# Kernel tuning notes

Hardware: AMD Instinct MI355X
Metric: run time of the kernel (lower is better)

The kernel has to match this reference:

```python
import jax, jax.numpy as jnp
import numpy as np

DIM = 1024
HEADS = 16
EPS = 1e-5


def layer_norm(x, gamma, beta):
    mu = jnp.mean(x, axis=-1, keepdims=True)
    var = jnp.mean(jnp.square(x - mu), axis=-1, keepdims=True)
    return (x - mu) * jax.lax.rsqrt(var + EPS) * gamma + beta


def setup_inputs() -> dict:
    key = jax.random.key(0)
    ks = jax.random.split(key, 9)
    B, Nq, Nk = 8, 1024, 1024
    s = 1.0 / np.sqrt(DIM)
    return {
        "x": jax.random.normal(ks[0], (B, Nq, DIM), jnp.float32),
        "context": jax.random.normal(ks[1], (B, Nk, DIM), jnp.float32),
        "relative_position_bias": jax.random.normal(ks[2], (HEADS, Nq, Nk), jnp.float32),
        "Wq": jax.random.normal(ks[3], (DIM, DIM), jnp.float32) * s,
        "Wk": jax.random.normal(ks[4], (DIM, DIM), jnp.float32) * s,
        "Wv": jax.random.normal(ks[5], (DIM, DIM), jnp.float32) * s,
        "Wo": jax.random.normal(ks[6], (DIM, DIM), jnp.float32) * s,
        "bo": jnp.zeros((DIM,), jnp.float32),
        "gamma": jnp.ones((DIM,), jnp.float32),
        "beta": jnp.zeros((DIM,), jnp.float32),
    }


def reference(x, context, relative_position_bias, Wq, Wk, Wv, Wo, bo, gamma, beta):
    h = HEADS
    d = DIM // h
    scale = d ** -0.5
    xn = layer_norm(x, gamma, beta)
    cn = layer_norm(context, gamma, beta)
    B, Nq, _ = x.shape
    Nk = context.shape[1]
    # b n (h d) -> b h n d
    q = (xn @ Wq).reshape(B, Nq, h, d).transpose(0, 2, 1, 3)
    k = (cn @ Wk).reshape(B, Nk, h, d).transpose(0, 2, 1, 3)
    v = (cn @ Wv).reshape(B, Nk, h, d).transpose(0, 2, 1, 3)
    scores = jnp.einsum('bhid,bhjd->bhij', q, k) * scale
    scores = scores + relative_position_bias[None]
    attn = jax.nn.softmax(scores, axis=-1)
    out = jnp.einsum('bhij,bhjd->bhid', attn, v)
    out = out.transpose(0, 2, 1, 3).reshape(B, Nq, h * d)
    return out @ Wo + bo
```

## Files before the change

### kernel.cpp

```cpp
#include <hip/hip_runtime.h>
#include <hip/hip_bf16.h>
#include <stdint.h>

#define DIM   1024
#define HEADS 16
#define HD    64
#define NB    8
#define NTOK  1024
#define MROWS (NB*NTOK)

#define LOG2E 1.4426950408889634f
#define SCL   (0.125f * LOG2E)

typedef __attribute__((ext_vector_type(8))) _Float16 f16x8;
typedef __attribute__((ext_vector_type(4))) _Float16 f16x4;
typedef __attribute__((ext_vector_type(4))) float    f32x4;

typedef unsigned int uint_as1 __attribute__((address_space(1)));
typedef unsigned int uint_as3 __attribute__((address_space(3)));

__device__ __forceinline__ void gload16(const void* g, void* l) {
    __builtin_amdgcn_global_load_lds((const uint_as1*)g, (uint_as3*)l, 16, 0, 0);
}

__device__ __forceinline__ unsigned pkrtz(float a, float b) {
    auto h = __builtin_amdgcn_cvt_pkrtz(a, b);
    return __builtin_bit_cast(unsigned, h);
}

#if __has_builtin(__builtin_amdgcn_permlane32_swap)
__device__ __forceinline__ void swap32(unsigned& a, unsigned& b) {
    auto r = __builtin_amdgcn_permlane32_swap(a, b, false, false);
    a = r[0]; b = r[1];
}
#else
__device__ __forceinline__ void swap32(unsigned& a, unsigned& b) {
    unsigned as = (unsigned)__shfl_xor((int)a, 32, 64);
    unsigned bs = (unsigned)__shfl_xor((int)b, 32, 64);
    bool lo = ((threadIdx.x & 63) < 32);
    unsigned na = lo ? a : bs, nb = lo ? as : b;
    a = na; b = nb;
}
#endif
#if __has_builtin(__builtin_amdgcn_permlane16_swap)
__device__ __forceinline__ void swap16(unsigned& a, unsigned& b) {
    auto r = __builtin_amdgcn_permlane16_swap(a, b, false, false);
    a = r[0]; b = r[1];
}
#else
__device__ __forceinline__ void swap16(unsigned& a, unsigned& b) {
    unsigned as = (unsigned)__shfl_xor((int)a, 16, 64);
    unsigned bs = (unsigned)__shfl_xor((int)b, 16, 64);
    bool ev = ((threadIdx.x & 16) == 0);
    unsigned na = ev ? a : bs, nb = ev ? as : b;
    a = na; b = nb;
}
#endif
__device__ __forceinline__ float redsum32(float x) {
    unsigned a = __builtin_bit_cast(unsigned, x), b = a;
    swap32(a, b);
    return __builtin_bit_cast(float, a) + __builtin_bit_cast(float, b);
}
__device__ __forceinline__ float redsum16(float x) {
    unsigned a = __builtin_bit_cast(unsigned, x), b = a;
    swap16(a, b);
    return __builtin_bit_cast(float, a) + __builtin_bit_cast(float, b);
}

__global__ __launch_bounds__(256) void ln_kernel(const float* __restrict__ x,
                                                 const float* __restrict__ ctx,
                                                 const float* __restrict__ gamma,
                                                 const float* __restrict__ beta,
                                                 _Float16* __restrict__ xn,
                                                 _Float16* __restrict__ cn) {
    int row = blockIdx.x;
    const float* src; _Float16* dst;
    if (row < MROWS) { src = x + (size_t)row * DIM;          dst = xn + (size_t)row * DIM; }
    else             { int r = row - MROWS;
                       src = ctx + (size_t)r * DIM;          dst = cn + (size_t)r * DIM; }
    int t = threadIdx.x;
    float4 v = *(const float4*)(src + t * 4);
    float s  = v.x + v.y + v.z + v.w;
    float s2 = v.x*v.x + v.y*v.y + v.z*v.z + v.w*v.w;
    #pragma unroll
    for (int o = 32; o; o >>= 1) { s += __shfl_xor(s, o, 64); s2 += __shfl_xor(s2, o, 64); }
    __shared__ float red[8];
    int w = t >> 6, l = t & 63;
    if (l == 0) { red[w] = s; red[4 + w] = s2; }
    __syncthreads();
    s  = red[0] + red[1] + red[2] + red[3];
    s2 = red[4] + red[5] + red[6] + red[7];
    float mu   = s * (1.0f / DIM);
    float rstd = rsqrtf(s2 * (1.0f / DIM) - mu * mu + 1e-5f);
    float4 g  = *(const float4*)(gamma + t * 4);
    float4 bb = *(const float4*)(beta  + t * 4);
    f16x4 o;
    o[0] = (_Float16)((v.x - mu) * rstd * g.x + bb.x);
    o[1] = (_Float16)((v.y - mu) * rstd * g.y + bb.y);
    o[2] = (_Float16)((v.z - mu) * rstd * g.z + bb.z);
    o[3] = (_Float16)((v.w - mu) * rstd * g.w + bb.w);
    *(f16x4*)(dst + t * 4) = o;
}

__global__ __launch_bounds__(256) void biasconv_kernel(const float* __restrict__ bias,
                                                       _Float16* __restrict__ bias2) {
    size_t i = ((size_t)blockIdx.x * 256 + threadIdx.x) * 8;
    float4 a = *(const float4*)(bias + i);
    float4 b = *(const float4*)(bias + i + 4);
    f16x8 o;
    o[0] = (_Float16)(a.x * LOG2E); o[1] = (_Float16)(a.y * LOG2E);
    o[2] = (_Float16)(a.z * LOG2E); o[3] = (_Float16)(a.w * LOG2E);
    o[4] = (_Float16)(b.x * LOG2E); o[5] = (_Float16)(b.y * LOG2E);
    o[6] = (_Float16)(b.z * LOG2E); o[7] = (_Float16)(b.w * LOG2E);
    *(f16x8*)(bias2 + i) = o;
}

__global__ __launch_bounds__(256) void wtrans_kernel(const float* __restrict__ Wq, const float* __restrict__ Wk,
                                                     const float* __restrict__ Wv, const float* __restrict__ Wo,
                                                     _Float16* __restrict__ Tq, _Float16* __restrict__ Tk,
                                                     _Float16* __restrict__ Tv, _Float16* __restrict__ To) {
    __shared__ float tile[32][33];
    int m = blockIdx.z;
    const float* W = (m == 0) ? Wq : (m == 1) ? Wk : (m == 2) ? Wv : Wo;
    _Float16*    T = (m == 0) ? Tq : (m == 1) ? Tk : (m == 2) ? Tv : To;
    int j0 = blockIdx.x * 32, k0 = blockIdx.y * 32;
    int tx = threadIdx.x, ty = threadIdx.y;
    #pragma unroll
    for (int i = 0; i < 4; i++) tile[ty + i*8][tx] = W[(size_t)(k0 + ty + i*8) * DIM + j0 + tx];
    __syncthreads();
    #pragma unroll
    for (int i = 0; i < 4; i++) T[(size_t)(j0 + ty + i*8) * DIM + k0 + tx] = (_Float16)tile[tx][ty + i*8];
}

template<int MODE>
__global__ __launch_bounds__(256) void gemm_bt(const _Float16* __restrict__ A,
                                               const _Float16* __restrict__ BT,
                                               void* __restrict__ Cout,
                                               void* __restrict__ Cout2,
                                               const float* __restrict__ bias) {
    __shared__ _Float16 As[128 * 64];
    __shared__ _Float16 Bs[128 * 64];
    const int K = DIM;
    int m0 = blockIdx.x * 128, n0 = blockIdx.y * 128;
    int t = threadIdx.x, w = t >> 6, l = t & 63;
    int wr = w >> 1, wc = w & 1, ln = l & 15, qtr = l >> 4;
    f32x4 acc[4][4] = {};
    int srow = w * 8 + (l >> 3);
    int cg   = (l & 7) ^ (srow & 7);
    const _Float16* Ag = A  + (size_t)(m0 + srow) * K + cg * 8;
    const _Float16* Bg = BT + (size_t)(n0 + srow) * K + cg * 8;
    for (int kt = 0; kt < K; kt += 64) {
        #pragma unroll
        for (int p = 0; p < 4; p++) {
            gload16(Ag + (size_t)(p * 32) * K, &As[(p * 32 + w * 8) * 64]);
            gload16(Bg + (size_t)(p * 32) * K, &Bs[(p * 32 + w * 8) * 64]);
        }
        Ag += 64; Bg += 64;
        __syncthreads();
        #pragma unroll
        for (int kk = 0; kk < 2; kk++) {
            f16x8 af[4], bfr[4];
            #pragma unroll
            for (int r = 0; r < 4; r++)
                af[r]  = *(const f16x8*)&As[(wr * 64 + r * 16 + ln) * 64 + (((qtr + kk*4) ^ (ln & 7)) * 8)];
            #pragma unroll
            for (int c = 0; c < 4; c++)
                bfr[c] = *(const f16x8*)&Bs[(wc * 64 + c * 16 + ln) * 64 + (((qtr + kk*4) ^ (ln & 7)) * 8)];
            #pragma unroll
            for (int r = 0; r < 4; r++)
                #pragma unroll
                for (int c = 0; c < 4; c++)
                    acc[r][c] = __builtin_amdgcn_mfma_f32_16x16x32_f16(af[r], bfr[c], acc[r][c], 0, 0, 0);
        }
        __syncthreads();
    }
    #pragma unroll
    for (int r = 0; r < 4; r++)
        #pragma unroll
        for (int c = 0; c < 4; c++) {
            int gn = n0 + wc * 64 + c * 16 + ln;
            #pragma unroll
            for (int q = 0; q < 4; q++) {
                int gm = m0 + wr * 64 + r * 16 + qtr * 4 + q;
                float v = acc[r][c][q];
                if constexpr (MODE == 0 || MODE == 1) {
                    int b = gm >> 10, n = gm & 1023, h = gn >> 6, d = gn & 63;
                    float sc = (MODE == 1) ? SCL : 1.0f;
                    ((_Float16*)Cout)[(((size_t)(b * HEADS + h) * NTOK + n) << 6) + d] = (_Float16)(v * sc);
                } else if constexpr (MODE == 2) {
                    int b = gm >> 10, n = gm & 1023, h = gn >> 6, d = gn & 63;
                    ((_Float16*)Cout)[(((size_t)(b * HEADS + h) * HD + d) << 10) + n] = (_Float16)v;
                } else if constexpr (MODE == 4) {
                    int b = gm >> 10, n = gm & 1023;
                    if (gn < 1024) {
                        int h = gn >> 6, d = gn & 63;
                        ((_Float16*)Cout)[(((size_t)(b * HEADS + h) * NTOK + n) << 6) + d] = (_Float16)v;
                    } else {
                        int g2 = gn - 1024, h = g2 >> 6, d = g2 & 63;
                        ((_Float16*)Cout2)[(((size_t)(b * HEADS + h) * HD + d) << 10) + n] = (_Float16)v;
                    }
                } else {
                    ((float*)Cout)[(size_t)gm * DIM + gn] = v + bias[gn];
                }
            }
        }
}

__global__ __launch_bounds__(256) void attn_kernel(const _Float16* __restrict__ qb,
                                                   const _Float16* __restrict__ kb,
                                                   const _Float16* __restrict__ vt,
                                                   const _Float16* __restrict__ bias2,
                                                   _Float16* __restrict__ ao) {
    __shared__ _Float16 Kt[2][64 * 64];
    __shared__ _Float16 Vs[2][64 * 64];
    int bid = blockIdx.x;
    int rem = bid >> 3;
    int h = (bid & 7) * 2 + (rem & 1);
    int b = (rem >> 1) & 7;
    int qt = rem >> 4;
    int q0 = qt * 64;
    int t = threadIdx.x, w = t >> 6, l = t & 63, ln = l & 15, qtr = l >> 4;
    const _Float16* qbase = qb + (size_t)(b * HEADS + h) * NTOK * HD;
    const _Float16* kbase = kb + (size_t)(b * HEADS + h) * NTOK * HD;
    const _Float16* vbase = vt + (size_t)(b * HEADS + h) * HD * NTOK;
    const _Float16* bbase = bias2 + ((size_t)h * NTOK + q0 + w * 16) * NTOK;

    f16x8 qfr[2];
    #pragma unroll
    for (int ks = 0; ks < 2; ks++)
        qfr[ks] = *(const f16x8*)&qbase[(size_t)(q0 + w*16 + ln) * HD + ks*32 + qtr*8];

#define STAGE(BUF, J0) do {                                                     \
        int rb_ = w * 16;                                                       \
        _Float16* kl_ = &Kt[BUF][rb_ * 64];                                     \
        _Float16* vl_ = &Vs[BUF][rb_ * 64];                                     \
        int r_ = rb_ + (l >> 3); int cg_ = (l & 7) ^ (r_ & 7);                  \
        gload16(kbase + (size_t)((J0) + r_) * HD + cg_ * 8, kl_);               \
        gload16(vbase + (size_t)r_ * NTOK + (J0) + cg_ * 8, vl_);               \
        r_ += 8; cg_ = (l & 7) ^ (r_ & 7);                                      \
        gload16(kbase + (size_t)((J0) + r_) * HD + cg_ * 8, kl_ + 8 * 64);      \
        gload16(vbase + (size_t)r_ * NTOK + (J0) + cg_ * 8, vl_ + 8 * 64);      \
    } while (0)

#define LOADB(DST, TT) do {                                                     \
        _Pragma("unroll")                                                       \
        for (int r_ = 0; r_ < 4; r_++)                                          \
            DST[r_] = *(const f16x4*)&bbase[(size_t)ln * NTOK                   \
                                            + (TT)*64 + qtr*4 + r_*16];         \
    } while (0)

    STAGE(0, 0);
    f16x4 bpp[2][4];
    LOADB(bpp[0], 0);
    __syncthreads();

    float l_part = 0.f;
    f32x4 acc[4] = {};

    #pragma unroll 2
    for (int tt = 0; tt < 16; tt++) {
        int cur = tt & 1;
        if (tt < 15) { STAGE(cur ^ 1, (tt + 1) * 64); LOADB(bpp[cur ^ 1], tt + 1); }

        f32x4 st2[4];
        #pragma unroll
        for (int r = 0; r < 4; r++) {
            f16x4 bb = bpp[cur][r];
            f32x4 ci = {(float)bb[0], (float)bb[1], (float)bb[2], (float)bb[3]};
            st2[r] = ci;
        }
        __builtin_amdgcn_s_setprio(1);
        #pragma unroll
        for (int r = 0; r < 4; r++) {
            int row = r * 16 + ln;
            #pragma unroll
            for (int ks = 0; ks < 2; ks++) {
                f16x8 kf = *(const f16x8*)&Kt[cur][row * 64 + (((qtr + ks*4) ^ (ln & 7)) * 8)];
                st2[r] = __builtin_amdgcn_mfma_f32_16x16x32_f16(kf, qfr[ks], st2[r], 0, 0, 0);
            }
        }
        __builtin_amdgcn_s_setprio(0);

        float sig = 0.f;
        unsigned pk2[4][2];
        #pragma unroll
        for (int r = 0; r < 4; r++) {
            float p0 = exp2f(st2[r][0]);
            float p1 = exp2f(st2[r][1]);
            float p2 = exp2f(st2[r][2]);
            float p3 = exp2f(st2[r][3]);
            sig += (p0 + p1) + (p2 + p3);
            pk2[r][0] = pkrtz(p0, p1);
            pk2[r][1] = pkrtz(p2, p3);
        }
        l_part += sig;

        f16x8 pfr[2];
        #pragma unroll
        for (int ks = 0; ks < 2; ks++) {
            unsigned pw[4];
            #pragma unroll
            for (int c = 0; c < 2; c++) {
                unsigned U = pk2[2*ks][c], T = pk2[2*ks + 1][c];
                swap32(U, T);
                swap16(U, T);
                pw[c]     = U;
                pw[2 + c] = T;
            }
            pfr[ks] = __builtin_bit_cast(f16x8, *(const uint4*)pw);
        }

        __builtin_amdgcn_s_setprio(1);
        #pragma unroll
        for (int dg = 0; dg < 4; dg++) {
            int row = dg * 16 + ln;
            #pragma unroll
            for (int ks = 0; ks < 2; ks++) {
                f16x8 vf = *(const f16x8*)&Vs[cur][row * 64 + (((qtr + ks*4) ^ (ln & 7)) * 8)];
                acc[dg] = __builtin_amdgcn_mfma_f32_16x16x32_f16(pfr[ks], vf, acc[dg], 0, 0, 0);
            }
        }
        __builtin_amdgcn_s_setprio(0);
        __syncthreads();
    }

    float inv = 1.0f / redsum16(redsum32(l_part));
    float invm[4];
    #pragma unroll
    for (int m = 0; m < 4; m++) invm[m] = __shfl(inv, (l & 48) | (qtr * 4 + m), 64);
    size_t rowb = (size_t)b * NTOK + q0 + w * 16 + qtr * 4;
    #pragma unroll
    for (int dg = 0; dg < 4; dg++)
        #pragma unroll
        for (int m = 0; m < 4; m++)
            ao[(rowb + m) * DIM + h * HD + dg * 16 + ln] = (_Float16)(acc[dg][m] * invm[m]);
#undef STAGE
#undef LOADB
}

extern "C" void kernel_launch(void* const* d_in, const int* in_sizes, int n_in,
                              void* d_out, int out_size, void* d_ws, size_t ws_size,
                              hipStream_t stream) {
    const float* x     = (const float*)d_in[0];
    const float* ctx   = (const float*)d_in[1];
    const float* bias  = (const float*)d_in[2];
    const float* Wq    = (const float*)d_in[3];
    const float* Wk    = (const float*)d_in[4];
    const float* Wv    = (const float*)d_in[5];
    const float* Wo    = (const float*)d_in[6];
    const float* bo    = (const float*)d_in[7];
    const float* gamma = (const float*)d_in[8];
    const float* beta  = (const float*)d_in[9];
    float* out = (float*)d_out;

    _Float16* ws  = (_Float16*)d_ws;
    _Float16* xn  = ws;
    _Float16* cn  = xn  + (size_t)MROWS * DIM;
    _Float16* wqT = cn  + (size_t)MROWS * DIM;
    _Float16* wkT = wqT + (size_t)DIM * DIM;
    _Float16* wvT = wkT + (size_t)DIM * DIM;
    _Float16* woT = wvT + (size_t)DIM * DIM;
    _Float16* qbf = woT + (size_t)DIM * DIM;
    _Float16* kbf = qbf + (size_t)MROWS * DIM;
    _Float16* vtb = kbf + (size_t)MROWS * DIM;
    _Float16* aob = vtb + (size_t)MROWS * DIM;
    _Float16* bias2 = ws;

    ln_kernel<<<dim3(2 * MROWS), dim3(256), 0, stream>>>(x, ctx, gamma, beta, xn, cn);
    wtrans_kernel<<<dim3(32, 32, 4), dim3(32, 8), 0, stream>>>(Wq, Wk, Wv, Wo, wqT, wkT, wvT, woT);
    gemm_bt<1><<<dim3(64, 8), dim3(256), 0, stream>>>(xn, wqT, qbf, nullptr, nullptr);
    gemm_bt<4><<<dim3(64, 16), dim3(256), 0, stream>>>(cn, wkT, kbf, vtb, nullptr);
    biasconv_kernel<<<dim3(8192), dim3(256), 0, stream>>>(bias, bias2);
    attn_kernel<<<dim3(NB * HEADS * 16), dim3(256), 0, stream>>>(qbf, kbf, vtb, bias2, aob);
    gemm_bt<3><<<dim3(64, 8), dim3(256), 0, stream>>>(aob, woT, out, nullptr, bo);
}
```

Before: 233.2 us.

## Merge prep kernels, fuse QKV projections, read fp32 bias directly in attention

Layer norm and weight transpose-conversion now run in a single launch. The Q, K and V projections run as one launch whose grid is split by mode. The separate bias-to-fp16 conversion kernel is removed: the attention kernel now loads the fp32 relative position bias directly and scales it by log2(e) in registers. This cuts kernel launches and one full pass over the 64 MB bias array. In exchange, attention reads twice as many bias bytes per tile, which can hurt its memory bandwidth.

Measured after the change: 227.3 us. 1.03x faster.

```diff
diff --git a/kernel.cpp b/kernel.cpp
--- a/kernel.cpp
+++ b/kernel.cpp
@@ -67,77 +67,135 @@
     return __builtin_bit_cast(float, a) + __builtin_bit_cast(float, b);
 }
 
-__global__ __launch_bounds__(256) void ln_kernel(const float* __restrict__ x,
-                                                 const float* __restrict__ ctx,
-                                                 const float* __restrict__ gamma,
-                                                 const float* __restrict__ beta,
-                                                 _Float16* __restrict__ xn,
-                                                 _Float16* __restrict__ cn) {
-    int row = blockIdx.x;
-    const float* src; _Float16* dst;
-    if (row < MROWS) { src = x + (size_t)row * DIM;          dst = xn + (size_t)row * DIM; }
-    else             { int r = row - MROWS;
-                       src = ctx + (size_t)r * DIM;          dst = cn + (size_t)r * DIM; }
+__global__ __launch_bounds__(256) void prep_kernel(const float* __restrict__ x,
+                                                   const float* __restrict__ ctx,
+                                                   const float* __restrict__ gamma,
+                                                   const float* __restrict__ beta,
+                                                   _Float16* __restrict__ xn,
+                                                   _Float16* __restrict__ cn,
+                                                   const float* __restrict__ Wq, const float* __restrict__ Wk,
+                                                   const float* __restrict__ Wv, const float* __restrict__ Wo,
+                                                   _Float16* __restrict__ Tq, _Float16* __restrict__ Tk,
+                                                   _Float16* __restrict__ Tv, _Float16* __restrict__ To) {
+    __shared__ float redm[8];
+    __shared__ float tile[32][33];
+    int bid = blockIdx.x;
     int t = threadIdx.x;
-    float4 v = *(const float4*)(src + t * 4);
-    float s  = v.x + v.y + v.z + v.w;
-    float s2 = v.x*v.x + v.y*v.y + v.z*v.z + v.w*v.w;
+    if (bid < 2 * MROWS) {
+        int row = bid;
+        const float* src; _Float16* dst;
+        if (row < MROWS) { src = x + (size_t)row * DIM;   dst = xn + (size_t)row * DIM; }
+        else             { int r = row - MROWS;
+                           src = ctx + (size_t)r * DIM;   dst = cn + (size_t)r * DIM; }
+        float4 v = *(const float4*)(src + t * 4);
+        float s  = v.x + v.y + v.z + v.w;
+        float s2 = v.x*v.x + v.y*v.y + v.z*v.z + v.w*v.w;
+        #pragma unroll
+        for (int o = 32; o; o >>= 1) { s += __shfl_xor(s, o, 64); s2 += __shfl_xor(s2, o, 64); }
+        int w = t >> 6, l = t & 63;
+        if (l == 0) { redm[w] = s; redm[4 + w] = s2; }
+        __syncthreads();
+        s  = redm[0] + redm[1] + redm[2] + redm[3];
+        s2 = redm[4] + redm[5] + redm[6] + redm[7];
+        float mu   = s * (1.0f / DIM);
+        float rstd = rsqrtf(s2 * (1.0f / DIM) - mu * mu + 1e-5f);
+        float4 g  = *(const float4*)(gamma + t * 4);
+        float4 bb = *(const float4*)(beta  + t * 4);
+        f16x4 o;
+        o[0] = (_Float16)((v.x - mu) * rstd * g.x + bb.x);
+        o[1] = (_Float16)((v.y - mu) * rstd * g.y + bb.y);
+        o[2] = (_Float16)((v.z - mu) * rstd * g.z + bb.z);
+        o[3] = (_Float16)((v.w - mu) * rstd * g.w + bb.w);
+        *(f16x4*)(dst + t * 4) = o;
+    } else {
+        int fid = bid - 2 * MROWS;
+        int m = fid >> 10;
+        int rem = fid & 1023;
+        int j0 = (rem & 31) * 32, k0 = (rem >> 5) * 32;
+        const float* W = (m == 0) ? Wq : (m == 1) ? Wk : (m == 2) ? Wv : Wo;
+        _Float16*    T = (m == 0) ? Tq : (m == 1) ? Tk : (m == 2) ? Tv : To;
+        int tx = t & 31, ty = t >> 5;
+        #pragma unroll
+        for (int i = 0; i < 4; i++) tile[ty + i*8][tx] = W[(size_t)(k0 + ty + i*8) * DIM + j0 + tx];
+        __syncthreads();
+        #pragma unroll
+        for (int i = 0; i < 4; i++) T[(size_t)(j0 + ty + i*8) * DIM + k0 + tx] = (_Float16)tile[tx][ty + i*8];
+    }
+}
+
+__global__ __launch_bounds__(256) void gemm_qkv(const _Float16* __restrict__ xn,
+                                                const _Float16* __restrict__ cn,
+                                                const _Float16* __restrict__ wqT,
+                                                const _Float16* __restrict__ wkT,
+                                                const _Float16* __restrict__ wvT,
+                                                _Float16* __restrict__ qbf,
+                                                _Float16* __restrict__ kbf,
+                                                _Float16* __restrict__ vtb) {
+    __shared__ _Float16 As[128 * 64];
+    __shared__ _Float16 Bs[128 * 64];
+    const int K = DIM;
+    int mode = blockIdx.y >> 3;
+    int n0 = (blockIdx.y & 7) * 128;
+    int m0 = blockIdx.x * 128;
+    const _Float16* A  = (mode == 0) ? xn : cn;
+    const _Float16* BT = (mode == 0) ? wqT : (mode == 1) ? wkT : wvT;
+    int t = threadIdx.x, w = t >> 6, l = t & 63;
+    int wr = w >> 1, wc = w & 1, ln = l & 15, qtr = l >> 4;
+    f32x4 acc[4][4] = {};
+    int srow = w * 8 + (l >> 3);
+    int cg   = (l & 7) ^ (srow & 7);
+    const _Float16* Ag = A  + (size_t)(m0 + srow) * K + cg * 8;
+    const _Float16* Bg = BT + (size_t)(n0 + srow) * K + cg * 8;
+    for (int kt = 0; kt < K; kt += 64) {
+        #pragma unroll
+        for (int p = 0; p < 4; p++) {
+            gload16(Ag + (size_t)(p * 32) * K, &As[(p * 32 + w * 8) * 64]);
+            gload16(Bg + (size_t)(p * 32) * K, &Bs[(p * 32 + w * 8) * 64]);
+        }
+        Ag += 64; Bg += 64;
+        __syncthreads();
+        #pragma unroll
+        for (int kk = 0; kk < 2; kk++) {
+            f16x8 af[4], bfr[4];
+            #pragma unroll
+            for (int r = 0; r < 4; r++)
+                af[r]  = *(const f16x8*)&As[(wr * 64 + r * 16 + ln) * 64 + (((qtr + kk*4) ^ (ln & 7)) * 8)];
+            #pragma unroll
+            for (int c = 0; c < 4; c++)
+                bfr[c] = *(const f16x8*)&Bs[(wc * 64 + c * 16 + ln) * 64 + (((qtr + kk*4) ^ (ln & 7)) * 8)];
+            #pragma unroll
+            for (int r = 0; r < 4; r++)
+                #pragma unroll
+                for (int c = 0; c < 4; c++)
+                    acc[r][c] = __builtin_amdgcn_mfma_f32_16x16x32_f16(af[r], bfr[c], acc[r][c], 0, 0, 0);
+        }
+        __syncthreads();
+    }
     #pragma unroll
-    for (int o = 32; o; o >>= 1) { s += __shfl_xor(s, o, 64); s2 += __shfl_xor(s2, o, 64); }
-    __shared__ float red[8];
-    int w = t >> 6, l = t & 63;
-    if (l == 0) { red[w] = s; red[4 + w] = s2; }
-    __syncthreads();
-    s  = red[0] + red[1] + red[2] + red[3];
-    s2 = red[4] + red[5] + red[6] + red[7];
-    float mu   = s * (1.0f / DIM);
-    float rstd = rsqrtf(s2 * (1.0f / DIM) - mu * mu + 1e-5f);
-    float4 g  = *(const float4*)(gamma + t * 4);
-    float4 bb = *(const float4*)(beta  + t * 4);
-    f16x4 o;
-    o[0] = (_Float16)((v.x - mu) * rstd * g.x + bb.x);
-    o[1] = (_Float16)((v.y - mu) * rstd * g.y + bb.y);
-    o[2] = (_Float16)((v.z - mu) * rstd * g.z + bb.z);
-    o[3] = (_Float16)((v.w - mu) * rstd * g.w + bb.w);
-    *(f16x4*)(dst + t * 4) = o;
-}
-
-__global__ __launch_bounds__(256) void biasconv_kernel(const float* __restrict__ bias,
-                                                       _Float16* __restrict__ bias2) {
-    size_t i = ((size_t)blockIdx.x * 256 + threadIdx.x) * 8;
-    float4 a = *(const float4*)(bias + i);
-    float4 b = *(const float4*)(bias + i + 4);
-    f16x8 o;
-    o[0] = (_Float16)(a.x * LOG2E); o[1] = (_Float16)(a.y * LOG2E);
-    o[2] = (_Float16)(a.z * LOG2E); o[3] = (_Float16)(a.w * LOG2E);
-    o[4] = (_Float16)(b.x * LOG2E); o[5] = (_Float16)(b.y * LOG2E);
-    o[6] = (_Float16)(b.z * LOG2E); o[7] = (_Float16)(b.w * LOG2E);
-    *(f16x8*)(bias2 + i) = o;
-}
-
-__global__ __launch_bounds__(256) void wtrans_kernel(const float* __restrict__ Wq, const float* __restrict__ Wk,
-                                                     const float* __restrict__ Wv, const float* __restrict__ Wo,
-                                                     _Float16* __restrict__ Tq, _Float16* __restrict__ Tk,
-                                                     _Float16* __restrict__ Tv, _Float16* __restrict__ To) {
-    __shared__ float tile[32][33];
-    int m = blockIdx.z;
-    const float* W = (m == 0) ? Wq : (m == 1) ? Wk : (m == 2) ? Wv : Wo;
-    _Float16*    T = (m == 0) ? Tq : (m == 1) ? Tk : (m == 2) ? Tv : To;
-    int j0 = blockIdx.x * 32, k0 = blockIdx.y * 32;
-    int tx = threadIdx.x, ty = threadIdx.y;
-    #pragma unroll
-    for (int i = 0; i < 4; i++) tile[ty + i*8][tx] = W[(size_t)(k0 + ty + i*8) * DIM + j0 + tx];
-    __syncthreads();
-    #pragma unroll
-    for (int i = 0; i < 4; i++) T[(size_t)(j0 + ty + i*8) * DIM + k0 + tx] = (_Float16)tile[tx][ty + i*8];
-}
-
-template<int MODE>
-__global__ __launch_bounds__(256) void gemm_bt(const _Float16* __restrict__ A,
-                                               const _Float16* __restrict__ BT,
-                                               void* __restrict__ Cout,
-                                               void* __restrict__ Cout2,
-                                               const float* __restrict__ bias) {
+    for (int r = 0; r < 4; r++)
+        #pragma unroll
+        for (int c = 0; c < 4; c++) {
+            int gn = n0 + wc * 64 + c * 16 + ln;
+            int h = gn >> 6, d = gn & 63;
+            #pragma unroll
+            for (int q = 0; q < 4; q++) {
+                int gm = m0 + wr * 64 + r * 16 + qtr * 4 + q;
+                int b = gm >> 10, n = gm & 1023;
+                float v = acc[r][c][q];
+                if (mode == 0)
+                    qbf[(((size_t)(b * HEADS + h) * NTOK + n) << 6) + d] = (_Float16)(v * SCL);
+                else if (mode == 1)
+                    kbf[(((size_t)(b * HEADS + h) * NTOK + n) << 6) + d] = (_Float16)v;
+                else
+                    vtb[(((size_t)(b * HEADS + h) * HD + d) << 10) + n] = (_Float16)v;
+            }
+        }
+}
+
+__global__ __launch_bounds__(256) void gemm_out(const _Float16* __restrict__ A,
+                                                const _Float16* __restrict__ BT,
+                                                float* __restrict__ Cout,
+                                                const float* __restrict__ bias) {
     __shared__ _Float16 As[128 * 64];
     __shared__ _Float16 Bs[128 * 64];
     const int K = DIM;
@@ -179,29 +237,11 @@
         #pragma unroll
         for (int c = 0; c < 4; c++) {
             int gn = n0 + wc * 64 + c * 16 + ln;
+            float bv = bias[gn];
             #pragma unroll
             for (int q = 0; q < 4; q++) {
                 int gm = m0 + wr * 64 + r * 16 + qtr * 4 + q;
-                float v = acc[r][c][q];
-                if constexpr (MODE == 0 || MODE == 1) {
-                    int b = gm >> 10, n = gm & 1023, h = gn >> 6, d = gn & 63;
-                    float sc = (MODE == 1) ? SCL : 1.0f;
-                    ((_Float16*)Cout)[(((size_t)(b * HEADS + h) * NTOK + n) << 6) + d] = (_Float16)(v * sc);
-                } else if constexpr (MODE == 2) {
-                    int b = gm >> 10, n = gm & 1023, h = gn >> 6, d = gn & 63;
-                    ((_Float16*)Cout)[(((size_t)(b * HEADS + h) * HD + d) << 10) + n] = (_Float16)v;
-                } else if constexpr (MODE == 4) {
-                    int b = gm >> 10, n = gm & 1023;
-                    if (gn < 1024) {
-                        int h = gn >> 6, d = gn & 63;
-                        ((_Float16*)Cout)[(((size_t)(b * HEADS + h) * NTOK + n) << 6) + d] = (_Float16)v;
-                    } else {
-                        int g2 = gn - 1024, h = g2 >> 6, d = g2 & 63;
-                        ((_Float16*)Cout2)[(((size_t)(b * HEADS + h) * HD + d) << 10) + n] = (_Float16)v;
-                    }
-                } else {
-                    ((float*)Cout)[(size_t)gm * DIM + gn] = v + bias[gn];
-                }
+                Cout[(size_t)gm * DIM + gn] = acc[r][c][q] + bv;
             }
         }
 }
@@ -209,7 +249,7 @@
 __global__ __launch_bounds__(256) void attn_kernel(const _Float16* __restrict__ qb,
                                                    const _Float16* __restrict__ kb,
                                                    const _Float16* __restrict__ vt,
-                                                   const _Float16* __restrict__ bias2,
+                                                   const float* __restrict__ bias,
                                                    _Float16* __restrict__ ao) {
     __shared__ _Float16 Kt[2][64 * 64];
     __shared__ _Float16 Vs[2][64 * 64];
@@ -223,7 +263,7 @@
     const _Float16* qbase = qb + (size_t)(b * HEADS + h) * NTOK * HD;
     const _Float16* kbase = kb + (size_t)(b * HEADS + h) * NTOK * HD;
     const _Float16* vbase = vt + (size_t)(b * HEADS + h) * HD * NTOK;
-    const _Float16* bbase = bias2 + ((size_t)h * NTOK + q0 + w * 16) * NTOK;
+    const float*    bbase = bias + ((size_t)h * NTOK + q0 + w * 16) * NTOK;
 
     f16x8 qfr[2];
     #pragma unroll
@@ -245,12 +285,12 @@
 #define LOADB(DST, TT) do {                                                     \
         _Pragma("unroll")                                                       \
         for (int r_ = 0; r_ < 4; r_++)                                          \
-            DST[r_] = *(const f16x4*)&bbase[(size_t)ln * NTOK                   \
-                                            + (TT)*64 + qtr*4 + r_*16];         \
+            DST[r_] = *(const float4*)&bbase[(size_t)ln * NTOK                  \
+                                             + (TT)*64 + qtr*4 + r_*16];        \
     } while (0)
 
     STAGE(0, 0);
-    f16x4 bpp[2][4];
+    float4 bpp[2][4];
     LOADB(bpp[0], 0);
     __syncthreads();
 
@@ -265,8 +305,8 @@
         f32x4 st2[4];
         #pragma unroll
         for (int r = 0; r < 4; r++) {
-            f16x4 bb = bpp[cur][r];
-            f32x4 ci = {(float)bb[0], (float)bb[1], (float)bb[2], (float)bb[3]};
+            float4 bb = bpp[cur][r];
+            f32x4 ci = {bb.x * LOG2E, bb.y * LOG2E, bb.z * LOG2E, bb.w * LOG2E};
             st2[r] = ci;
         }
         __builtin_amdgcn_s_setprio(1);
@@ -364,13 +404,10 @@
     _Float16* kbf = qbf + (size_t)MROWS * DIM;
     _Float16* vtb = kbf + (size_t)MROWS * DIM;
     _Float16* aob = vtb + (size_t)MROWS * DIM;
-    _Float16* bias2 = ws;
-
-    ln_kernel<<<dim3(2 * MROWS), dim3(256), 0, stream>>>(x, ctx, gamma, beta, xn, cn);
-    wtrans_kernel<<<dim3(32, 32, 4), dim3(32, 8), 0, stream>>>(Wq, Wk, Wv, Wo, wqT, wkT, wvT, woT);
-    gemm_bt<1><<<dim3(64, 8), dim3(256), 0, stream>>>(xn, wqT, qbf, nullptr, nullptr);
-    gemm_bt<4><<<dim3(64, 16), dim3(256), 0, stream>>>(cn, wkT, kbf, vtb, nullptr);
-    biasconv_kernel<<<dim3(8192), dim3(256), 0, stream>>>(bias, bias2);
-    attn_kernel<<<dim3(NB * HEADS * 16), dim3(256), 0, stream>>>(qbf, kbf, vtb, bias2, aob);
-    gemm_bt<3><<<dim3(64, 8), dim3(256), 0, stream>>>(aob, woT, out, nullptr, bo);
-}
+
+    prep_kernel<<<dim3(2 * MROWS + 4096), dim3(256), 0, stream>>>(
+        x, ctx, gamma, beta, xn, cn, Wq, Wk, Wv, Wo, wqT, wkT, wvT, woT);
+    gemm_qkv<<<dim3(64, 24), dim3(256), 0, stream>>>(xn, cn, wqT, wkT, wvT, qbf, kbf, vtb);
+    attn_kernel<<<dim3(NB * HEADS * 16), dim3(256), 0, stream>>>(qbf, kbf, vtb, bias, aob);
+    gemm_out<<<dim3(64, 8), dim3(256), 0, stream>>>(aob, woT, out, bo);
+}
```
